# Optimization experiments

Hardware: AMD Instinct MI355X
Metric: run time of the kernel (lower is better)

## Reference

```python
import jax, jax.numpy as jnp
import numpy as np
import math

B, L, D = 2, 2048, 512
D_INNER, D_STATE, D_CONV = 2 * D, 16, 4
DT_RANK = math.ceil(D / 16)  # 32


def setup_inputs() -> dict:
    key = jax.random.key(0)
    ks = jax.random.split(key, 9)
    s = 0.02
    x = jax.random.normal(ks[0], (B, L, D), dtype=jnp.float32)
    W_in = jax.random.normal(ks[1], (D, 2 * D_INNER), dtype=jnp.float32) * s
    conv_w = jax.random.normal(ks[2], (D_INNER, D_CONV), dtype=jnp.float32) * s
    conv_b = jnp.zeros((D_INNER,), dtype=jnp.float32)
    W_x = jax.random.normal(ks[3], (D_INNER, DT_RANK + 2 * D_STATE), dtype=jnp.float32) * s
    W_dt = jax.random.normal(ks[4], (DT_RANK, D_INNER), dtype=jnp.float32) * s
    b_dt = jax.random.normal(ks[5], (D_INNER,), dtype=jnp.float32) * s
    # S4D-real init: A = -[1..d_state] per channel
    A_log = jnp.log(jnp.broadcast_to(jnp.arange(1, D_STATE + 1, dtype=jnp.float32), (D_INNER, D_STATE)))
    D_param = jnp.ones((D_INNER,), dtype=jnp.float32)
    W_out = jax.random.normal(ks[6], (D_INNER, D), dtype=jnp.float32) * s
    return {"x": x, "W_in": W_in, "conv_w": conv_w, "conv_b": conv_b,
            "W_x": W_x, "W_dt": W_dt, "b_dt": b_dt, "A_log": A_log,
            "D_param": D_param, "W_out": W_out}


def _mamba(x, W_in, conv_w, conv_b, W_x, W_dt, b_dt, A_log, D_param, W_out):
    # in_proj -> [u, z]
    xz = jnp.einsum('bld,de->ble', x, W_in)
    u, z = jnp.split(xz, 2, axis=-1)  # each (B, L, d_inner)
    # depthwise causal conv1d along L
    u_c = jnp.transpose(u, (0, 2, 1))  # (B, d_inner, L)
    kern = conv_w[:, None, :]          # (d_inner, 1, d_conv)
    u_c = jax.lax.conv_general_dilated(
        u_c, kern, window_strides=(1,), padding=[(D_CONV - 1, 0)],
        feature_group_count=D_INNER,
        dimension_numbers=('NCH', 'OIH', 'NCH')) + conv_b[None, :, None]
    u = jax.nn.silu(jnp.transpose(u_c, (0, 2, 1)))  # (B, L, d_inner)
    # input-dependent dt, B, C
    x_dbl = jnp.einsum('bld,de->ble', u, W_x)
    dt_r = x_dbl[..., :DT_RANK]
    Bm = x_dbl[..., DT_RANK:DT_RANK + D_STATE]          # (B, L, d_state)
    Cm = x_dbl[..., DT_RANK + D_STATE:]                  # (B, L, d_state)
    dt = jax.nn.softplus(jnp.einsum('blr,rd->bld', dt_r, W_dt) + b_dt)  # (B, L, d_inner)
    A = -jnp.exp(A_log)  # (d_inner, d_state)

    def step(h, inp):
        dt_t, B_t, C_t, u_t = inp  # (B,d_inner), (B,d_state), (B,d_state), (B,d_inner)
        dA = jnp.exp(dt_t[:, :, None] * A)                      # (B, d_inner, d_state)
        h = h * dA + (dt_t * u_t)[:, :, None] * B_t[:, None, :]
        y = jnp.einsum('bds,bs->bd', h, C_t)
        return h, y

    h0 = jnp.zeros((B, D_INNER, D_STATE), dtype=x.dtype)
    xs = (jnp.transpose(dt, (1, 0, 2)), jnp.transpose(Bm, (1, 0, 2)),
          jnp.transpose(Cm, (1, 0, 2)), jnp.transpose(u, (1, 0, 2)))
    _, ys = jax.lax.scan(step, h0, xs)
    y = jnp.transpose(ys, (1, 0, 2)) + u * D_param  # (B, L, d_inner)
    y = y * jax.nn.silu(z)
    return jnp.einsum('bld,de->ble', y, W_out)


def reference(x, W_in, conv_w, conv_b, W_x, W_dt, b_dt, A_log, D_param, W_out):
    # MambaLayer.forward (eval): out = x + drop_path(mamba(x)); drop_path == Identity at eval
    return x + _mamba(x, W_in, conv_w, conv_b, W_x, W_dt, b_dt, A_log, D_param, W_out)
```

## Files before the change

kernel.cpp:

```cpp
#include <hip/hip_runtime.h>
#include <math.h>

#define BB 2
#define LL 2048
#define DD 512
#define DIN 1024
#define DXZ 2048
#define DSTATE 16
#define DTRANK 32
#define NDBL 64
#define ML (BB*LL)
#define LC2 64
#define NCH2 (LL/LC2)
#define CP 68

typedef __bf16 bf16_t;
typedef bf16_t bf16x8 __attribute__((ext_vector_type(8)));
typedef bf16_t bf16x4 __attribute__((ext_vector_type(4)));
typedef float f32x4 __attribute__((ext_vector_type(4)));

#define GBK 32
#define GBKP 40

__device__ __forceinline__ float fast_silu(float x) {
  return x * __builtin_amdgcn_rcpf(1.f + __builtin_amdgcn_exp2f(-1.44269504f * x));
}

template <int TM, int TN, int MODE, int CT, int OB>
__launch_bounds__(256)
__global__ void gemm_mfma(const bf16_t* __restrict__ A,
                          const bf16_t* __restrict__ Bt,
                          void* __restrict__ Cv, int ldc,
                          int M, int N, int K,
                          const float* __restrict__ aux) {
  __shared__ __align__(16) bf16_t As[TM * GBKP];
  __shared__ __align__(16) bf16_t Bs[TN * GBKP];
  float* C = (float*)Cv;
  bf16_t* Cb = (bf16_t*)Cv;
  const int tid = threadIdx.x;
  const int wid = tid >> 6, lane = tid & 63;
  const int q = lane >> 4, ln = lane & 15;
  constexpr int WM = TM / 2, WN = TN / 2;
  constexpr int FM = WM / 16, FN = WN / 16;
  const int wm = (wid >> 1) * WM, wn = (wid & 1) * WN;
  const int mBase = blockIdx.y * TM, nBase = blockIdx.x * TN;

  f32x4 acc[FM][FN] = {};

  for (int k0 = 0; k0 < K; k0 += GBK) {
#pragma unroll
    for (int i = 0; i < TM * GBK / (256 * 8); i++) {
      const int slot = tid + i * 256;
      const int m = slot >> 2, k8 = (slot & 3) * 8;
      *(bf16x8*)&As[m * GBKP + k8] =
          *(const bf16x8*)&A[(size_t)(mBase + m) * K + k0 + k8];
    }
#pragma unroll
    for (int i = 0; i < TN * GBK / (256 * 8); i++) {
      const int slot = tid + i * 256;
      const int n = slot >> 2, k8 = (slot & 3) * 8;
      *(bf16x8*)&Bs[n * GBKP + k8] =
          *(const bf16x8*)&Bt[(size_t)(nBase + n) * K + k0 + k8];
    }
    __syncthreads();
    bf16x8 af[FM], bfr[FN];
#pragma unroll
    for (int i = 0; i < FM; i++)
      af[i] = *(const bf16x8*)&As[(wm + i * 16 + ln) * GBKP + q * 8];
#pragma unroll
    for (int j = 0; j < FN; j++)
      bfr[j] = *(const bf16x8*)&Bs[(wn + j * 16 + ln) * GBKP + q * 8];
#pragma unroll
    for (int i = 0; i < FM; i++)
#pragma unroll
      for (int j = 0; j < FN; j++)
        acc[i][j] = __builtin_amdgcn_mfma_f32_16x16x32_bf16(
            af[i], bfr[j], acc[i][j], 0, 0, 0);
    __syncthreads();
  }

#pragma unroll
  for (int i = 0; i < FM; i++) {
    const int m0 = mBase + wm + i * 16 + q * 4;
#pragma unroll
    for (int j = 0; j < FN; j++) {
      const int n = nBase + wn + j * 16 + ln;
      if (CT == 1) {
        if (OB == 1) {
          bf16x4 o = {(bf16_t)acc[i][j][0], (bf16_t)acc[i][j][1],
                      (bf16_t)acc[i][j][2], (bf16_t)acc[i][j][3]};
          *(bf16x4*)&Cb[(size_t)n * ldc + m0] = o;
        } else {
          *(f32x4*)&C[(size_t)n * ldc + m0] = acc[i][j];
        }
      } else {
#pragma unroll
        for (int r = 0; r < 4; r++) {
          float v = acc[i][j][r];
          if (MODE == 2) v += aux[(size_t)(m0 + r) * ldc + n];
          C[(size_t)(m0 + r) * ldc + n] = v;
        }
      }
    }
  }
}

__global__ void cast_bf16(const float* __restrict__ in, bf16_t* __restrict__ out,
                          int n4) {
  const int i = blockIdx.x * 256 + threadIdx.x;
  if (i >= n4) return;
  const float4 v = ((const float4*)in)[i];
  bf16x4 o = {(bf16_t)v.x, (bf16_t)v.y, (bf16_t)v.z, (bf16_t)v.w};
  ((bf16x4*)out)[i] = o;
}

template <typename TIN>
__launch_bounds__(256)
__global__ void transpose_cast(const TIN* __restrict__ in, bf16_t* __restrict__ out,
                               int R, int C) {
  __shared__ float T[64][65];
  const int t = threadIdx.x;
  const int rB = blockIdx.y * 64, cB = blockIdx.x * 64;
  {
    const int r = t >> 4, c4 = (t & 15) * 4;
#pragma unroll
    for (int i = 0; i < 4; i++) {
      const TIN* src = &in[(size_t)(rB + r + i * 16) * C + cB + c4];
      float v0, v1, v2, v3;
      if (sizeof(TIN) == 4) {
        const float4 v = *(const float4*)src;
        v0 = v.x; v1 = v.y; v2 = v.z; v3 = v.w;
      } else {
        const bf16x4 v = *(const bf16x4*)src;
        v0 = (float)v[0]; v1 = (float)v[1]; v2 = (float)v[2]; v3 = (float)v[3];
      }
      T[r + i * 16][c4] = v0;
      T[r + i * 16][c4 + 1] = v1;
      T[r + i * 16][c4 + 2] = v2;
      T[r + i * 16][c4 + 3] = v3;
    }
  }
  __syncthreads();
  {
    const int c = t >> 2;
#pragma unroll
    for (int i = 0; i < 4; i++) {
      const int r0 = (t & 3) * 16 + i * 4;
      bf16x4 o = {(bf16_t)T[r0][c], (bf16_t)T[r0 + 1][c],
                  (bf16_t)T[r0 + 2][c], (bf16_t)T[r0 + 3][c]};
      *(bf16x4*)&out[(size_t)(cB + c) * R + rB + r0] = o;
    }
  }
}

template <int MODE, int AT, int CT>
__launch_bounds__(256)
__global__ void gemm_tiled(const float* __restrict__ A, int lda,
                           const float* __restrict__ B, int ldb,
                           float* __restrict__ C, int ldc,
                           int M, int N, int K,
                           const float* __restrict__ aux) {
  __shared__ float As[16][68];
  __shared__ float Bs[16][68];

  const int tid = threadIdx.x;
  const int tx = tid & 15, ty = tid >> 4;
  const int mBase = blockIdx.y * 64;
  const int nBase = blockIdx.x * 64;

  float acc[4][4] = {};

  for (int k0 = 0; k0 < K; k0 += 16) {
#pragma unroll
    for (int i = 0; i < 4; i++) {
      int idx = tid + i * 256;
      if (AT == 0) {
        int m = idx >> 4, kk = idx & 15;
        As[kk][m] = A[(size_t)(mBase + m) * lda + k0 + kk];
      } else {
        int kk = idx >> 6, m = idx & 63;
        As[kk][m] = A[(size_t)(k0 + kk) * lda + mBase + m];
      }
    }
#pragma unroll
    for (int i = 0; i < 4; i++) {
      int idx = tid + i * 256;
      int kk = idx >> 6, n = idx & 63;
      Bs[kk][n] = B[(size_t)(k0 + kk) * ldb + nBase + n];
    }
    __syncthreads();
#pragma unroll
    for (int kk = 0; kk < 16; kk++) {
      const float4 a4 = *reinterpret_cast<const float4*>(&As[kk][ty * 4]);
      const float4 b4 = *reinterpret_cast<const float4*>(&Bs[kk][tx * 4]);
      const float a[4] = {a4.x, a4.y, a4.z, a4.w};
      const float b[4] = {b4.x, b4.y, b4.z, b4.w};
#pragma unroll
      for (int i = 0; i < 4; i++)
#pragma unroll
        for (int j = 0; j < 4; j++) acc[i][j] = fmaf(a[i], b[j], acc[i][j]);
    }
    __syncthreads();
  }

  if (CT == 0) {
#pragma unroll
    for (int i = 0; i < 4; i++) {
      const int m = mBase + ty * 4 + i;
      const int n0 = nBase + tx * 4;
      float v[4];
#pragma unroll
      for (int j = 0; j < 4; j++) {
        float x = acc[i][j];
        if (MODE == 1) {
          x += aux[n0 + j];
          x = (x > 20.f) ? x
              : 0.69314718f * __builtin_amdgcn_logf(
                    1.f + __builtin_amdgcn_exp2f(x * 1.44269504f));
        }
        v[j] = x;
      }
      *reinterpret_cast<float4*>(&C[(size_t)m * ldc + n0]) =
          make_float4(v[0], v[1], v[2], v[3]);
    }
  } else {
    const int m0 = mBase + ty * 4;
#pragma unroll
    for (int j = 0; j < 4; j++) {
      const int n = nBase + tx * 4 + j;
      float v[4];
#pragma unroll
      for (int i = 0; i < 4; i++) {
        float x = acc[i][j];
        if (MODE == 1) {
          x += aux[n];
          x = (x > 20.f) ? x
              : 0.69314718f * __builtin_amdgcn_logf(
                    1.f + __builtin_amdgcn_exp2f(x * 1.44269504f));
        }
        v[i] = x;
      }
      *reinterpret_cast<float4*>(&C[(size_t)n * ldc + m0]) =
          make_float4(v[0], v[1], v[2], v[3]);
    }
  }
}

__launch_bounds__(256)
__global__ void conv_silu_T(const bf16_t* __restrict__ xzTb,
                            const float* __restrict__ conv_w,
                            const float* __restrict__ conv_b,
                            float* __restrict__ uT) {
  const int idx = blockIdx.x * 256 + threadIdx.x;
  const int d = idx >> 10;
  const int ml0 = (idx & 1023) * 4;
  const int l0 = ml0 & (LL - 1);
  const bf16_t* row = xzTb + (size_t)d * ML + ml0;
  const bf16x4 Bv4 = *(const bf16x4*)row;
  bf16x4 Av4 = {(bf16_t)0.f, (bf16_t)0.f, (bf16_t)0.f, (bf16_t)0.f};
  if (l0 != 0) Av4 = *(const bf16x4*)(row - 4);
  const float Ay = (float)Av4[1], Az = (float)Av4[2], Aw = (float)Av4[3];
  const float Bx = (float)Bv4[0], By = (float)Bv4[1], Bz = (float)Bv4[2],
              Bw = (float)Bv4[3];
  const float w0 = conv_w[d * 4 + 0], w1 = conv_w[d * 4 + 1];
  const float w2 = conv_w[d * 4 + 2], w3 = conv_w[d * 4 + 3];
  const float bias = conv_b[d];
  float o[4];
  o[0] = bias + w0 * Ay + w1 * Az + w2 * Aw + w3 * Bx;
  o[1] = bias + w0 * Az + w1 * Aw + w2 * Bx + w3 * By;
  o[2] = bias + w0 * Aw + w1 * Bx + w2 * By + w3 * Bz;
  o[3] = bias + w0 * Bx + w1 * By + w2 * Bz + w3 * Bw;
#pragma unroll
  for (int i = 0; i < 4; i++) o[i] = fast_silu(o[i]);
  *reinterpret_cast<float4*>(uT + (size_t)d * ML + ml0) =
      make_float4(o[0], o[1], o[2], o[3]);
}

__launch_bounds__(256, 3)
__global__ void scan_fused4(const float* __restrict__ dtT,
                            const float* __restrict__ uT,
                            const bf16_t* __restrict__ xzTb,
                            bf16_t* __restrict__ yTb,
                            const float* __restrict__ xdbl,
                            const float* __restrict__ A_log,
                            const float* __restrict__ D_param) {
  __shared__ float dt_s[2][NCH2 * CP];
  __shared__ float u_s[2][NCH2 * CP];
  __shared__ float Pc[2][NCH2][DSTATE];
  __shared__ float Hc[2][NCH2][DSTATE];
  __shared__ float Al2s[2][DSTATE];

  const int tid = threadIdx.x;
  const int half = tid >> 7;
  const int ht = tid & 127;
  const int c = blockIdx.x * 2 + half;
  const int b = c >> 10, d = c & (DIN - 1);
  const size_t rowoff = (size_t)d * ML + (size_t)b * LL;
  const float* dtrow = dtT + rowoff;
  const float* urow  = uT + rowoff;
  const bf16_t* zrow = xzTb + (size_t)(DIN + d) * ML + (size_t)b * LL;
  bf16_t* yrow = yTb + rowoff;

  float* dts = dt_s[half];
  float* us  = u_s[half];

#pragma unroll
  for (int i = 0; i < 4; i++) {
    const int idx = (ht + i * 128) * 4;
    const int la = (idx >> 6) * CP + (idx & 63);
    *(float4*)&dts[la] = *(const float4*)&dtrow[idx];
    *(float4*)&us[la]  = *(const float4*)&urow[idx];
  }
  if (ht < DSTATE)
    Al2s[half][ht] = -expf(A_log[d * DSTATE + ht]) * 1.44269504f;

  const int ch = ht >> 2, q = ht & 3;
  const int s0 = q * 4;
  const float* BC = xdbl + ((size_t)b * LL + (size_t)ch * LC2) * NDBL + DTRANK + s0;
  const float Dp = D_param[d];
  __syncthreads();

  float Al2[4];
#pragma unroll
  for (int k = 0; k < 4; k++) Al2[k] = Al2s[half][s0 + k];

  {
    float* dp = dts + ch * CP;
    float* up = us + ch * CP;
    float h0 = 0.f, h1 = 0.f, h2 = 0.f, h3 = 0.f, sdt = 0.f;
    float4 Bcur[4], Ccur[4];
#pragma unroll
    for (int i = 0; i < 4; i++) {
      Bcur[i] = *(const float4*)(BC + (size_t)i * NDBL);
      Ccur[i] = *(const float4*)(BC + (size_t)i * NDBL + DSTATE);
    }
    for (int g = 0; g < 16; g++) {
      const int gn = (g < 15) ? g + 1 : 15;
      float4 Bn[4], Cn[4];
#pragma unroll
      for (int i = 0; i < 4; i++) {
        Bn[i] = *(const float4*)(BC + (size_t)(gn * 4 + i) * NDBL);
        Cn[i] = *(const float4*)(BC + (size_t)(gn * 4 + i) * NDBL + DSTATE);
      }
#pragma unroll
      for (int i = 0; i < 4; i++) {
        const int l = g * 4 + i;
        const float dtv = dp[l];
        const float uv = up[l];
        const float dtu = dtv * uv;
        sdt += dtv;
        const float e0 = __builtin_amdgcn_exp2f(dtv * Al2[0]);
        const float e1 = __builtin_amdgcn_exp2f(dtv * Al2[1]);
        const float e2 = __builtin_amdgcn_exp2f(dtv * Al2[2]);
        const float e3 = __builtin_amdgcn_exp2f(dtv * Al2[3]);
        h0 = fmaf(h0, e0, dtu * Bcur[i].x);
        h1 = fmaf(h1, e1, dtu * Bcur[i].y);
        h2 = fmaf(h2, e2, dtu * Bcur[i].z);
        h3 = fmaf(h3, e3, dtu * Bcur[i].w);
        float p = fmaf(h0, Ccur[i].x,
                  fmaf(h1, Ccur[i].y, fmaf(h2, Ccur[i].z, h3 * Ccur[i].w)));
        p += __int_as_float(__builtin_amdgcn_ds_swizzle(__float_as_int(p), 0x041F));
        p += __int_as_float(__builtin_amdgcn_ds_swizzle(__float_as_int(p), 0x081F));
        if (q == i) {
          up[l] = p + uv * Dp;
          dp[l] = sdt;
        }
      }
#pragma unroll
      for (int i = 0; i < 4; i++) { Bcur[i] = Bn[i]; Ccur[i] = Cn[i]; }
    }
    *(float4*)&Pc[half][ch][s0] = make_float4(
        __builtin_amdgcn_exp2f(Al2[0] * sdt), __builtin_amdgcn_exp2f(Al2[1] * sdt),
        __builtin_amdgcn_exp2f(Al2[2] * sdt), __builtin_amdgcn_exp2f(Al2[3] * sdt));
    *(float4*)&Hc[half][ch][s0] = make_float4(h0, h1, h2, h3);
  }
  __syncthreads();

  if (ht < DSTATE) {
    float h = 0.f;
#pragma unroll
    for (int k = 0; k < NCH2; k++) {
      const float Pv = Pc[half][k][ht], Hv = Hc[half][k][ht];
      Pc[half][k][ht] = h;
      h = fmaf(h, Pv, Hv);
    }
  }
  __syncthreads();

  {
    float A16[16];
#pragma unroll
    for (int s = 0; s < 16; s++) A16[s] = Al2s[half][s];
#pragma unroll 4
    for (int i = 0; i < 16; i++) {
      const int l = ht + i * 128;
      const int ck = l >> 6;
      const int la = ck * CP + (l & 63);
      const float sdt = dts[la];
      const float* Crow = xdbl + ((size_t)b * LL + l) * NDBL + DTRANK + DSTATE;
      const float4 C0 = *(const float4*)(Crow + 0);
      const float4 C1 = *(const float4*)(Crow + 4);
      const float4 C2 = *(const float4*)(Crow + 8);
      const float4 C3 = *(const float4*)(Crow + 12);
      const float4 g0 = *(const float4*)&Pc[half][ck][0];
      const float4 g1 = *(const float4*)&Pc[half][ck][4];
      const float4 g2 = *(const float4*)&Pc[half][ck][8];
      const float4 g3 = *(const float4*)&Pc[half][ck][12];
      float corr = 0.f;
      corr = fmaf(C0.x * g0.x, __builtin_amdgcn_exp2f(A16[0] * sdt), corr);
      corr = fmaf(C0.y * g0.y, __builtin_amdgcn_exp2f(A16[1] * sdt), corr);
      corr = fmaf(C0.z * g0.z, __builtin_amdgcn_exp2f(A16[2] * sdt), corr);
      corr = fmaf(C0.w * g0.w, __builtin_amdgcn_exp2f(A16[3] * sdt), corr);
      corr = fmaf(C1.x * g1.x, __builtin_amdgcn_exp2f(A16[4] * sdt), corr);
      corr = fmaf(C1.y * g1.y, __builtin_amdgcn_exp2f(A16[5] * sdt), corr);
      corr = fmaf(C1.z * g1.z, __builtin_amdgcn_exp2f(A16[6] * sdt), corr);
      corr = fmaf(C1.w * g1.w, __builtin_amdgcn_exp2f(A16[7] * sdt), corr);
      corr = fmaf(C2.x * g2.x, __builtin_amdgcn_exp2f(A16[8] * sdt), corr);
      corr = fmaf(C2.y * g2.y, __builtin_amdgcn_exp2f(A16[9] * sdt), corr);
      corr = fmaf(C2.z * g2.z, __builtin_amdgcn_exp2f(A16[10] * sdt), corr);
      corr = fmaf(C2.w * g2.w, __builtin_amdgcn_exp2f(A16[11] * sdt), corr);
      corr = fmaf(C3.x * g3.x, __builtin_amdgcn_exp2f(A16[12] * sdt), corr);
      corr = fmaf(C3.y * g3.y, __builtin_amdgcn_exp2f(A16[13] * sdt), corr);
      corr = fmaf(C3.z * g3.z, __builtin_amdgcn_exp2f(A16[14] * sdt), corr);
      corr = fmaf(C3.w * g3.w, __builtin_amdgcn_exp2f(A16[15] * sdt), corr);
      us[la] += corr;
    }
  }
  __syncthreads();

#pragma unroll
  for (int i = 0; i < 4; i++) {
    const int idx = (ht + i * 128) * 4;
    const int la = (idx >> 6) * CP + (idx & 63);
    const float4 y4 = *(const float4*)&us[la];
    const bf16x4 z4 = *(const bf16x4*)&zrow[idx];
    bf16x4 o = {(bf16_t)(y4.x * fast_silu((float)z4[0])),
                (bf16_t)(y4.y * fast_silu((float)z4[1])),
                (bf16_t)(y4.z * fast_silu((float)z4[2])),
                (bf16_t)(y4.w * fast_silu((float)z4[3]))};
    *(bf16x4*)&yrow[idx] = o;
  }
}

extern "C" void kernel_launch(void* const* d_in, const int* in_sizes, int n_in,
                              void* d_out, int out_size, void* d_ws, size_t ws_size,
                              hipStream_t stream) {
  const float* x      = (const float*)d_in[0];
  const float* W_in   = (const float*)d_in[1];
  const float* conv_w = (const float*)d_in[2];
  const float* conv_b = (const float*)d_in[3];
  const float* W_x    = (const float*)d_in[4];
  const float* W_dt   = (const float*)d_in[5];
  const float* b_dt   = (const float*)d_in[6];
  const float* A_log  = (const float*)d_in[7];
  const float* D_par  = (const float*)d_in[8];
  const float* W_out  = (const float*)d_in[9];
  float* out = (float*)d_out;

  const size_t MB = 1 << 20;
  char* ws = (char*)d_ws;
  bf16_t* xzTb = (bf16_t*)ws;
  float* uT    = (float*)(ws + 16 * MB);
  float* x_dbl = (float*)(ws + 32 * MB);
  float* dtT   = (float*)(ws + 33 * MB);
  bf16_t* u_b  = (bf16_t*)(ws + 49 * MB);
  bf16_t* y_b  = (bf16_t*)(ws + 49 * MB);
  bf16_t* yTb  = (bf16_t*)(ws + 57 * MB);
  bf16_t* x_b      = (bf16_t*)(ws + 65 * MB);
  bf16_t* W_inT_b  = (bf16_t*)(ws + 69 * MB);
  bf16_t* W_outT_b = (bf16_t*)(ws + 71 * MB);
  bf16_t* W_xT_b   = (bf16_t*)(ws + 72 * MB);

  cast_bf16<<<(ML * DD / 4) / 256, 256, 0, stream>>>(x, x_b, ML * DD / 4);
  transpose_cast<float><<<dim3(DXZ / 64, DD / 64), 256, 0, stream>>>(W_in, W_inT_b, DD, DXZ);
  transpose_cast<float><<<dim3(1, DIN / 64), 256, 0, stream>>>(W_x, W_xT_b, DIN, NDBL);
  transpose_cast<float><<<dim3(DD / 64, DIN / 64), 256, 0, stream>>>(W_out, W_outT_b, DIN, DD);

  gemm_mfma<128, 128, 0, 1, 1><<<dim3(DXZ / 128, ML / 128), 256, 0, stream>>>(
      x_b, W_inT_b, xzTb, ML, ML, DXZ, DD, nullptr);

  conv_silu_T<<<(DIN * (ML / 4)) / 256, 256, 0, stream>>>(xzTb, conv_w, conv_b, uT);

  transpose_cast<float><<<dim3(ML / 64, DIN / 64), 256, 0, stream>>>(uT, u_b, DIN, ML);

  gemm_mfma<64, 64, 0, 0, 0><<<dim3(1, ML / 64), 256, 0, stream>>>(
      u_b, W_xT_b, x_dbl, NDBL, ML, NDBL, DIN, nullptr);

  gemm_tiled<1, 0, 1><<<dim3(DIN / 64, ML / 64), 256, 0, stream>>>(
      x_dbl, NDBL, W_dt, DIN, dtT, ML, ML, DIN, DTRANK, b_dt);

  scan_fused4<<<BB * DIN / 2, 256, 0, stream>>>(dtT, uT, xzTb, yTb, x_dbl, A_log, D_par);

  transpose_cast<bf16_t><<<dim3(ML / 64, DIN / 64), 256, 0, stream>>>(yTb, y_b, DIN, ML);

  gemm_mfma<128, 64, 2, 0, 0><<<dim3(DD / 64, ML / 128), 256, 0, stream>>>(
      y_b, W_outT_b, out, DD, ML, DD, DIN, x);
}
```

Measured before the change: 234.6 us.

## Restructure scan into two-pass chunked form and split-K the x_dbl projection

The scan kernel now runs one channel per 128-thread block. A first pass computes per-chunk state and decay, then a carry pass, then a second pass that recomputes outputs from the correct initial state. This replaces the old correction pass with its 16 exp2 per element. dt is stored as bf16 and u and y are held in bf16 shared memory. The x_dbl projection moves from an MFMA GEMM on a transposed bf16 copy of u to a split-K fp32 tiled GEMM that reads the transposed u directly and accumulates with atomics after a memset, which removes a transpose and a weight cast. This adds a second sequential pass over each chunk and lowers the precision of the intermediates.

```diff
diff --git a/kernel.cpp b/kernel.cpp
--- a/kernel.cpp
+++ b/kernel.cpp
@@ -12,7 +12,7 @@
 #define ML (BB*LL)
 #define LC2 64
 #define NCH2 (LL/LC2)
-#define CP 68
+#define CPH 72
 
 typedef __bf16 bf16_t;
 typedef bf16_t bf16x8 __attribute__((ext_vector_type(8)));
@@ -153,24 +153,28 @@
   }
 }
 
-template <int MODE, int AT, int CT>
+template <int MODE, int AT, int CT, int OB>
 __launch_bounds__(256)
 __global__ void gemm_tiled(const float* __restrict__ A, int lda,
                            const float* __restrict__ B, int ldb,
-                           float* __restrict__ C, int ldc,
+                           void* __restrict__ Cv, int ldc,
                            int M, int N, int K,
                            const float* __restrict__ aux) {
   __shared__ float As[16][68];
   __shared__ float Bs[16][68];
+  float* C = (float*)Cv;
+  bf16_t* Cb = (bf16_t*)Cv;
 
   const int tid = threadIdx.x;
   const int tx = tid & 15, ty = tid >> 4;
   const int mBase = blockIdx.y * 64;
   const int nBase = blockIdx.x * 64;
+  const int kPer = K / gridDim.z;
+  const int kBeg = blockIdx.z * kPer;
 
   float acc[4][4] = {};
 
-  for (int k0 = 0; k0 < K; k0 += 16) {
+  for (int k0 = kBeg; k0 < kBeg + kPer; k0 += 16) {
 #pragma unroll
     for (int i = 0; i < 4; i++) {
       int idx = tid + i * 256;
@@ -208,20 +212,26 @@
     for (int i = 0; i < 4; i++) {
       const int m = mBase + ty * 4 + i;
       const int n0 = nBase + tx * 4;
-      float v[4];
-#pragma unroll
-      for (int j = 0; j < 4; j++) {
-        float x = acc[i][j];
-        if (MODE == 1) {
-          x += aux[n0 + j];
-          x = (x > 20.f) ? x
-              : 0.69314718f * __builtin_amdgcn_logf(
-                    1.f + __builtin_amdgcn_exp2f(x * 1.44269504f));
+      if (MODE == 3) {
+#pragma unroll
+        for (int j = 0; j < 4; j++)
+          atomicAdd(&C[(size_t)m * ldc + n0 + j], acc[i][j]);
+      } else {
+        float v[4];
+#pragma unroll
+        for (int j = 0; j < 4; j++) {
+          float x = acc[i][j];
+          if (MODE == 1) {
+            x += aux[n0 + j];
+            x = (x > 20.f) ? x
+                : 0.69314718f * __builtin_amdgcn_logf(
+                      1.f + __builtin_amdgcn_exp2f(x * 1.44269504f));
+          }
+          v[j] = x;
         }
-        v[j] = x;
-      }
-      *reinterpret_cast<float4*>(&C[(size_t)m * ldc + n0]) =
-          make_float4(v[0], v[1], v[2], v[3]);
+        *reinterpret_cast<float4*>(&C[(size_t)m * ldc + n0]) =
+            make_float4(v[0], v[1], v[2], v[3]);
+      }
     }
   } else {
     const int m0 = mBase + ty * 4;
@@ -240,8 +250,13 @@
         }
         v[i] = x;
       }
-      *reinterpret_cast<float4*>(&C[(size_t)n * ldc + m0]) =
-          make_float4(v[0], v[1], v[2], v[3]);
+      if (OB == 1) {
+        bf16x4 o = {(bf16_t)v[0], (bf16_t)v[1], (bf16_t)v[2], (bf16_t)v[3]};
+        *(bf16x4*)&Cb[(size_t)n * ldc + m0] = o;
+      } else {
+        *reinterpret_cast<float4*>(&C[(size_t)n * ldc + m0]) =
+            make_float4(v[0], v[1], v[2], v[3]);
+      }
     }
   }
 }
@@ -276,58 +291,106 @@
       make_float4(o[0], o[1], o[2], o[3]);
 }
 
-__launch_bounds__(256, 3)
-__global__ void scan_fused4(const float* __restrict__ dtT,
+__launch_bounds__(128, 4)
+__global__ void scan_fused5(const bf16_t* __restrict__ dtTb,
                             const float* __restrict__ uT,
                             const bf16_t* __restrict__ xzTb,
                             bf16_t* __restrict__ yTb,
                             const float* __restrict__ xdbl,
                             const float* __restrict__ A_log,
                             const float* __restrict__ D_param) {
-  __shared__ float dt_s[2][NCH2 * CP];
-  __shared__ float u_s[2][NCH2 * CP];
-  __shared__ float Pc[2][NCH2][DSTATE];
-  __shared__ float Hc[2][NCH2][DSTATE];
-  __shared__ float Al2s[2][DSTATE];
+  __shared__ bf16_t dt_s[NCH2 * CPH];
+  __shared__ bf16_t u_s[NCH2 * CPH];
+  __shared__ float Pc[NCH2][DSTATE];
+  __shared__ float Hc[NCH2][DSTATE];
 
   const int tid = threadIdx.x;
-  const int half = tid >> 7;
-  const int ht = tid & 127;
-  const int c = blockIdx.x * 2 + half;
+  const int c = blockIdx.x;
   const int b = c >> 10, d = c & (DIN - 1);
   const size_t rowoff = (size_t)d * ML + (size_t)b * LL;
-  const float* dtrow = dtT + rowoff;
-  const float* urow  = uT + rowoff;
+  const bf16_t* dtrow = dtTb + rowoff;
+  const float* urow = uT + rowoff;
   const bf16_t* zrow = xzTb + (size_t)(DIN + d) * ML + (size_t)b * LL;
   bf16_t* yrow = yTb + rowoff;
 
-  float* dts = dt_s[half];
-  float* us  = u_s[half];
-
+#pragma unroll
+  for (int i = 0; i < 2; i++) {
+    const int e = (tid + i * 128) * 8;
+    const int la = (e >> 6) * CPH + (e & 63);
+    *(bf16x8*)&dt_s[la] = *(const bf16x8*)&dtrow[e];
+  }
 #pragma unroll
   for (int i = 0; i < 4; i++) {
-    const int idx = (ht + i * 128) * 4;
-    const int la = (idx >> 6) * CP + (idx & 63);
-    *(float4*)&dts[la] = *(const float4*)&dtrow[idx];
-    *(float4*)&us[la]  = *(const float4*)&urow[idx];
-  }
-  if (ht < DSTATE)
-    Al2s[half][ht] = -expf(A_log[d * DSTATE + ht]) * 1.44269504f;
-
-  const int ch = ht >> 2, q = ht & 3;
+    const int e = (tid + i * 128) * 4;
+    const int la = (e >> 6) * CPH + (e & 63);
+    const float4 v = *(const float4*)&urow[e];
+    bf16x4 o = {(bf16_t)v.x, (bf16_t)v.y, (bf16_t)v.z, (bf16_t)v.w};
+    *(bf16x4*)&u_s[la] = o;
+  }
+
+  const int ch = tid >> 2, q = tid & 3;
   const int s0 = q * 4;
+  float Al2[4];
+#pragma unroll
+  for (int k = 0; k < 4; k++)
+    Al2[k] = -expf(A_log[d * DSTATE + s0 + k]) * 1.44269504f;
+  const bf16_t* dp = dt_s + ch * CPH;
+  bf16_t* up = u_s + ch * CPH;
   const float* BC = xdbl + ((size_t)b * LL + (size_t)ch * LC2) * NDBL + DTRANK + s0;
   const float Dp = D_param[d];
   __syncthreads();
 
-  float Al2[4];
-#pragma unroll
-  for (int k = 0; k < 4; k++) Al2[k] = Al2s[half][s0 + k];
-
   {
-    float* dp = dts + ch * CP;
-    float* up = us + ch * CP;
     float h0 = 0.f, h1 = 0.f, h2 = 0.f, h3 = 0.f, sdt = 0.f;
+    float4 Bcur[4];
+#pragma unroll
+    for (int i = 0; i < 4; i++)
+      Bcur[i] = *(const float4*)(BC + (size_t)i * NDBL);
+    for (int g = 0; g < 16; g++) {
+      const int gn = (g < 15) ? g + 1 : 15;
+      float4 Bn[4];
+#pragma unroll
+      for (int i = 0; i < 4; i++)
+        Bn[i] = *(const float4*)(BC + (size_t)(gn * 4 + i) * NDBL);
+#pragma unroll
+      for (int i = 0; i < 4; i++) {
+        const int l = g * 4 + i;
+        const float dtv = (float)dp[l];
+        const float dtu = dtv * (float)up[l];
+        sdt += dtv;
+        const float e0 = __builtin_amdgcn_exp2f(dtv * Al2[0]);
+        const float e1 = __builtin_amdgcn_exp2f(dtv * Al2[1]);
+        const float e2 = __builtin_amdgcn_exp2f(dtv * Al2[2]);
+        const float e3 = __builtin_amdgcn_exp2f(dtv * Al2[3]);
+        h0 = fmaf(h0, e0, dtu * Bcur[i].x);
+        h1 = fmaf(h1, e1, dtu * Bcur[i].y);
+        h2 = fmaf(h2, e2, dtu * Bcur[i].z);
+        h3 = fmaf(h3, e3, dtu * Bcur[i].w);
+      }
+#pragma unroll
+      for (int i = 0; i < 4; i++) Bcur[i] = Bn[i];
+    }
+    *(float4*)&Pc[ch][s0] = make_float4(
+        __builtin_amdgcn_exp2f(Al2[0] * sdt), __builtin_amdgcn_exp2f(Al2[1] * sdt),
+        __builtin_amdgcn_exp2f(Al2[2] * sdt), __builtin_amdgcn_exp2f(Al2[3] * sdt));
+    *(float4*)&Hc[ch][s0] = make_float4(h0, h1, h2, h3);
+  }
+  __syncthreads();
+
+  if (tid < DSTATE) {
+    float h = 0.f;
+#pragma unroll
+    for (int k = 0; k < NCH2; k++) {
+      const float Pv = Pc[k][tid], Hv = Hc[k][tid];
+      Pc[k][tid] = h;
+      h = fmaf(h, Pv, Hv);
+    }
+  }
+  __syncthreads();
+
+  {
+    const float4 H4 = *(const float4*)&Pc[ch][s0];
+    float h0 = H4.x, h1 = H4.y, h2 = H4.z, h3 = H4.w;
     float4 Bcur[4], Ccur[4];
 #pragma unroll
     for (int i = 0; i < 4; i++) {
@@ -345,10 +408,9 @@
 #pragma unroll
       for (int i = 0; i < 4; i++) {
         const int l = g * 4 + i;
-        const float dtv = dp[l];
-        const float uv = up[l];
+        const float dtv = (float)dp[l];
+        const float uv = (float)up[l];
         const float dtu = dtv * uv;
-        sdt += dtv;
         const float e0 = __builtin_amdgcn_exp2f(dtv * Al2[0]);
         const float e1 = __builtin_amdgcn_exp2f(dtv * Al2[1]);
         const float e2 = __builtin_amdgcn_exp2f(dtv * Al2[2]);
@@ -361,84 +423,25 @@
                   fmaf(h1, Ccur[i].y, fmaf(h2, Ccur[i].z, h3 * Ccur[i].w)));
         p += __int_as_float(__builtin_amdgcn_ds_swizzle(__float_as_int(p), 0x041F));
         p += __int_as_float(__builtin_amdgcn_ds_swizzle(__float_as_int(p), 0x081F));
-        if (q == i) {
-          up[l] = p + uv * Dp;
-          dp[l] = sdt;
-        }
+        if (q == i) up[l] = (bf16_t)(p + uv * Dp);
       }
 #pragma unroll
       for (int i = 0; i < 4; i++) { Bcur[i] = Bn[i]; Ccur[i] = Cn[i]; }
     }
-    *(float4*)&Pc[half][ch][s0] = make_float4(
-        __builtin_amdgcn_exp2f(Al2[0] * sdt), __builtin_amdgcn_exp2f(Al2[1] * sdt),
-        __builtin_amdgcn_exp2f(Al2[2] * sdt), __builtin_amdgcn_exp2f(Al2[3] * sdt));
-    *(float4*)&Hc[half][ch][s0] = make_float4(h0, h1, h2, h3);
   }
   __syncthreads();
 
-  if (ht < DSTATE) {
-    float h = 0.f;
-#pragma unroll
-    for (int k = 0; k < NCH2; k++) {
-      const float Pv = Pc[half][k][ht], Hv = Hc[half][k][ht];
-      Pc[half][k][ht] = h;
-      h = fmaf(h, Pv, Hv);
-    }
-  }
-  __syncthreads();
-
-  {
-    float A16[16];
-#pragma unroll
-    for (int s = 0; s < 16; s++) A16[s] = Al2s[half][s];
-#pragma unroll 4
-    for (int i = 0; i < 16; i++) {
-      const int l = ht + i * 128;
-      const int ck = l >> 6;
-      const int la = ck * CP + (l & 63);
-      const float sdt = dts[la];
-      const float* Crow = xdbl + ((size_t)b * LL + l) * NDBL + DTRANK + DSTATE;
-      const float4 C0 = *(const float4*)(Crow + 0);
-      const float4 C1 = *(const float4*)(Crow + 4);
-      const float4 C2 = *(const float4*)(Crow + 8);
-      const float4 C3 = *(const float4*)(Crow + 12);
-      const float4 g0 = *(const float4*)&Pc[half][ck][0];
-      const float4 g1 = *(const float4*)&Pc[half][ck][4];
-      const float4 g2 = *(const float4*)&Pc[half][ck][8];
-      const float4 g3 = *(const float4*)&Pc[half][ck][12];
-      float corr = 0.f;
-      corr = fmaf(C0.x * g0.x, __builtin_amdgcn_exp2f(A16[0] * sdt), corr);
-      corr = fmaf(C0.y * g0.y, __builtin_amdgcn_exp2f(A16[1] * sdt), corr);
-      corr = fmaf(C0.z * g0.z, __builtin_amdgcn_exp2f(A16[2] * sdt), corr);
-      corr = fmaf(C0.w * g0.w, __builtin_amdgcn_exp2f(A16[3] * sdt), corr);
-      corr = fmaf(C1.x * g1.x, __builtin_amdgcn_exp2f(A16[4] * sdt), corr);
-      corr = fmaf(C1.y * g1.y, __builtin_amdgcn_exp2f(A16[5] * sdt), corr);
-      corr = fmaf(C1.z * g1.z, __builtin_amdgcn_exp2f(A16[6] * sdt), corr);
-      corr = fmaf(C1.w * g1.w, __builtin_amdgcn_exp2f(A16[7] * sdt), corr);
-      corr = fmaf(C2.x * g2.x, __builtin_amdgcn_exp2f(A16[8] * sdt), corr);
-      corr = fmaf(C2.y * g2.y, __builtin_amdgcn_exp2f(A16[9] * sdt), corr);
-      corr = fmaf(C2.z * g2.z, __builtin_amdgcn_exp2f(A16[10] * sdt), corr);
-      corr = fmaf(C2.w * g2.w, __builtin_amdgcn_exp2f(A16[11] * sdt), corr);
-      corr = fmaf(C3.x * g3.x, __builtin_amdgcn_exp2f(A16[12] * sdt), corr);
-      corr = fmaf(C3.y * g3.y, __builtin_amdgcn_exp2f(A16[13] * sdt), corr);
-      corr = fmaf(C3.z * g3.z, __builtin_amdgcn_exp2f(A16[14] * sdt), corr);
-      corr = fmaf(C3.w * g3.w, __builtin_amdgcn_exp2f(A16[15] * sdt), corr);
-      us[la] += corr;
-    }
-  }
-  __syncthreads();
-
 #pragma unroll
   for (int i = 0; i < 4; i++) {
-    const int idx = (ht + i * 128) * 4;
-    const int la = (idx >> 6) * CP + (idx & 63);
-    const float4 y4 = *(const float4*)&us[la];
-    const bf16x4 z4 = *(const bf16x4*)&zrow[idx];
-    bf16x4 o = {(bf16_t)(y4.x * fast_silu((float)z4[0])),
-                (bf16_t)(y4.y * fast_silu((float)z4[1])),
-                (bf16_t)(y4.z * fast_silu((float)z4[2])),
-                (bf16_t)(y4.w * fast_silu((float)z4[3]))};
-    *(bf16x4*)&yrow[idx] = o;
+    const int e = (tid + i * 128) * 4;
+    const int la = (e >> 6) * CPH + (e & 63);
+    const bf16x4 y4 = *(const bf16x4*)&u_s[la];
+    const bf16x4 z4 = *(const bf16x4*)&zrow[e];
+    bf16x4 o = {(bf16_t)((float)y4[0] * fast_silu((float)z4[0])),
+                (bf16_t)((float)y4[1] * fast_silu((float)z4[1])),
+                (bf16_t)((float)y4[2] * fast_silu((float)z4[2])),
+                (bf16_t)((float)y4[3] * fast_silu((float)z4[3]))};
+    *(bf16x4*)&yrow[e] = o;
   }
 }
 
@@ -462,18 +465,15 @@
   bf16_t* xzTb = (bf16_t*)ws;
   float* uT    = (float*)(ws + 16 * MB);
   float* x_dbl = (float*)(ws + 32 * MB);
-  float* dtT   = (float*)(ws + 33 * MB);
-  bf16_t* u_b  = (bf16_t*)(ws + 49 * MB);
+  bf16_t* dtTb = (bf16_t*)(ws + 33 * MB);
+  bf16_t* yTb  = (bf16_t*)(ws + 41 * MB);
   bf16_t* y_b  = (bf16_t*)(ws + 49 * MB);
-  bf16_t* yTb  = (bf16_t*)(ws + 57 * MB);
-  bf16_t* x_b      = (bf16_t*)(ws + 65 * MB);
-  bf16_t* W_inT_b  = (bf16_t*)(ws + 69 * MB);
-  bf16_t* W_outT_b = (bf16_t*)(ws + 71 * MB);
-  bf16_t* W_xT_b   = (bf16_t*)(ws + 72 * MB);
+  bf16_t* x_b      = (bf16_t*)(ws + 57 * MB);
+  bf16_t* W_inT_b  = (bf16_t*)(ws + 61 * MB);
+  bf16_t* W_outT_b = (bf16_t*)(ws + 63 * MB);
 
   cast_bf16<<<(ML * DD / 4) / 256, 256, 0, stream>>>(x, x_b, ML * DD / 4);
   transpose_cast<float><<<dim3(DXZ / 64, DD / 64), 256, 0, stream>>>(W_in, W_inT_b, DD, DXZ);
-  transpose_cast<float><<<dim3(1, DIN / 64), 256, 0, stream>>>(W_x, W_xT_b, DIN, NDBL);
   transpose_cast<float><<<dim3(DD / 64, DIN / 64), 256, 0, stream>>>(W_out, W_outT_b, DIN, DD);
 
   gemm_mfma<128, 128, 0, 1, 1><<<dim3(DXZ / 128, ML / 128), 256, 0, stream>>>(
@@ -481,15 +481,14 @@
 
   conv_silu_T<<<(DIN * (ML / 4)) / 256, 256, 0, stream>>>(xzTb, conv_w, conv_b, uT);
 
-  transpose_cast<float><<<dim3(ML / 64, DIN / 64), 256, 0, stream>>>(uT, u_b, DIN, ML);
-
-  gemm_mfma<64, 64, 0, 0, 0><<<dim3(1, ML / 64), 256, 0, stream>>>(
-      u_b, W_xT_b, x_dbl, NDBL, ML, NDBL, DIN, nullptr);
-
-  gemm_tiled<1, 0, 1><<<dim3(DIN / 64, ML / 64), 256, 0, stream>>>(
-      x_dbl, NDBL, W_dt, DIN, dtT, ML, ML, DIN, DTRANK, b_dt);
-
-  scan_fused4<<<BB * DIN / 2, 256, 0, stream>>>(dtT, uT, xzTb, yTb, x_dbl, A_log, D_par);
+  hipMemsetAsync(x_dbl, 0, (size_t)ML * NDBL * 4, stream);
+  gemm_tiled<3, 1, 0, 0><<<dim3(1, ML / 64, 8), 256, 0, stream>>>(
+      uT, ML, W_x, NDBL, x_dbl, NDBL, ML, NDBL, DIN, nullptr);
+
+  gemm_tiled<1, 0, 1, 1><<<dim3(DIN / 64, ML / 64, 1), 256, 0, stream>>>(
+      x_dbl, NDBL, W_dt, DIN, dtTb, ML, ML, DIN, DTRANK, b_dt);
+
+  scan_fused5<<<BB * DIN, 128, 0, stream>>>(dtTb, uT, xzTb, yTb, x_dbl, A_log, D_par);
 
   transpose_cast<bf16_t><<<dim3(ML / 64, DIN / 64), 256, 0, stream>>>(yTb, y_b, DIN, ML);
 
```

After: 229.1 us. 1.02x faster.
